# Kernel tuning notes

Measured on AMD Instinct MI355X. Metric: run time of the kernel, lower is better.

## Reference

```python
import jax, jax.numpy as jnp
import numpy as np

EPS = 1e-9
TEMP = 1.0
TOP_K = 2


def setup_inputs() -> dict:
    key = jax.random.key(0)
    k1, k2, k3, k4 = jax.random.split(key, 4)
    B, T, D, DC, E = 8, 4096, 1024, 512, 64
    din = D + DC
    inputs = jax.random.normal(k1, (B, T, D), dtype=jnp.float32)
    cond = jax.random.normal(k2, (B, T, DC), dtype=jnp.float32)
    # CondRouterMLP params (bias=False): Linear(din -> 2*din), GELU, Linear(2*din -> E)
    W1 = jax.random.normal(k3, (2 * din, din), dtype=jnp.float32) / np.sqrt(din).astype(np.float32)
    W2 = jax.random.normal(k4, (E, 2 * din), dtype=jnp.float32) / np.sqrt(2 * din).astype(np.float32)
    return {"inputs": inputs, "cond": cond, "W1": W1, "W2": W2}


def reference(inputs, cond, W1, W2):
    B, T, D = inputs.shape
    # concat hidden states with condition, flatten tokens
    x = jnp.concatenate([inputs, cond], axis=-1).reshape(-1, D + cond.shape[-1])  # [N, din]
    h = jax.nn.gelu(x @ W1.T, approximate=False)          # [N, 2*din] (torch nn.GELU = exact erf)
    logits = h @ W2.T                                     # [N, E]
    logits = (logits - logits.max(axis=-1, keepdims=True)) / TEMP
    probs = jax.nn.softmax(logits, axis=-1) + EPS
    probs = jnp.clip(probs, EPS, 1.0 - EPS)               # [N, E]
    # eval-mode top-k selection
    top_v, top_i = jax.lax.top_k(probs, TOP_K)            # [N, k]
    N, E = probs.shape
    rows = jnp.arange(N)[:, None]
    router_mask = jnp.zeros_like(probs).at[rows, top_i].set(1.0)
    router_probs = jnp.zeros_like(probs).at[rows, top_i].set(top_v)
    router_probs = router_probs / router_probs.sum(axis=-1, keepdims=True)  # normalize=True
    return (
        router_mask.reshape(B, T, E),
        top_i.reshape(B, T, TOP_K),
        router_probs.reshape(B, T, E),
        probs.reshape(B, T, E),
    )
```

## Files before the change

### kernel.cpp

```cpp
#include <hip/hip_runtime.h>
#include <cmath>

#define N_TOK 32768
#define D0    1024
#define DCC   512
#define DIN   1536
#define JD    3072
#define NE    64
#define BM    128
#define BJ    512
#define NJC   (JD/BJ)
#define NIT   48
#define NTH   512
#define HS    36
#define EPSV  1e-9f

typedef _Float16 half8 __attribute__((ext_vector_type(8)));
typedef float    f32x4 __attribute__((ext_vector_type(4)));

#define SZ_A  16384
#define SZ_B  65536
#define OFF_A 0
#define OFF_B 32768
#define LDS_TOTAL 163840
#define OFF_H    0
#define OFF_LRED 73728
#define OFF_EPI  (73728 + 34816)

#define W1N   ((size_t)JD*DIN)
#define W2N   ((size_t)NE*JD)
#define XTN   ((size_t)N_TOK*DIN)
#define XT_G  (256*192*128)
#define W1T_G (192*3072)
#define W2T_G (384*64)

__device__ __forceinline__ f32x4 mfma16(half8 a, half8 b, f32x4 c) {
    return __builtin_amdgcn_mfma_f32_16x16x32_f16(a, b, c, 0, 0, 0);
}

__device__ __forceinline__ void split8(const float4 v0, const float4 v1, half8& hh, half8& hl) {
    float f[8] = {v0.x, v0.y, v0.z, v0.w, v1.x, v1.y, v1.z, v1.w};
    #pragma unroll
    for (int i = 0; i < 8; ++i) {
        _Float16 h = (_Float16)f[i];
        hh[i] = h;
        hl[i] = (_Float16)(f[i] - (float)h);
    }
}

__device__ __forceinline__ void gload16(const void* g, void* l) {
    __builtin_amdgcn_global_load_lds(
        (const __attribute__((address_space(1))) unsigned int*)g,
        (__attribute__((address_space(3))) unsigned int*)l, 16, 0, 0);
}

__global__ void presplit_w1t(const float* __restrict__ W1,
                             _Float16* __restrict__ hi, _Float16* __restrict__ lo) {
    int g = blockIdx.x * blockDim.x + threadIdx.x;
    if (g >= W1T_G) return;
    const int j  = g % JD;
    const int ko = g / JD;
    const float* src = W1 + (size_t)j * DIN + ko * 8;
    float4 v0 = *(const float4*)src;
    float4 v1 = *(const float4*)(src + 4);
    half8 h, l;
    split8(v0, v1, h, l);
    *(half8*)(hi + (size_t)g * 8) = h;
    *(half8*)(lo + (size_t)g * 8) = l;
}

__global__ void presplit_w2t(const float* __restrict__ W2,
                             _Float16* __restrict__ hi, _Float16* __restrict__ lo) {
    int g = blockIdx.x * blockDim.x + threadIdx.x;
    if (g >= W2T_G) return;
    const int e  = g & 63;
    const int jo = g >> 6;
    const float* src = W2 + (size_t)e * JD + jo * 8;
    float4 v0 = *(const float4*)src;
    float4 v1 = *(const float4*)(src + 4);
    half8 h, l;
    split8(v0, v1, h, l);
    *(half8*)(hi + (size_t)g * 8) = h;
    *(half8*)(lo + (size_t)g * 8) = l;
}

__global__ void presplit_xt(const float* __restrict__ inp, const float* __restrict__ cnd,
                            _Float16* __restrict__ hi, _Float16* __restrict__ lo) {
    int g = blockIdx.x * blockDim.x + threadIdx.x;
    if (g >= XT_G) return;
    const int r    = g & 127;
    const int ko   = (g >> 7) % 192;
    const int tile = g / (192 * 128);
    const int token = tile * 128 + r;
    const float* src = (ko < 128) ? (inp + (size_t)token * D0 + ko * 8)
                                  : (cnd + (size_t)token * DCC + (ko - 128) * 8);
    float4 v0 = *(const float4*)src;
    float4 v1 = *(const float4*)(src + 4);
    half8 h, l;
    split8(v0, v1, h, l);
    *(half8*)(hi + (size_t)g * 8) = h;
    *(half8*)(lo + (size_t)g * 8) = l;
}

__global__ __launch_bounds__(NTH, 1)
void router_v17(const _Float16* __restrict__ Xh, const _Float16* __restrict__ Xl,
                const _Float16* __restrict__ W1h, const _Float16* __restrict__ W1l,
                const _Float16* __restrict__ W2h, const _Float16* __restrict__ W2l,
                float* __restrict__ out_mask, float* __restrict__ out_topi,
                float* __restrict__ out_rp, float* __restrict__ out_probs)
{
    __shared__ __align__(16) char smem[LDS_TOTAL];

    const int tid  = threadIdx.x;
    const int lane = tid & 63;
    const int w    = tid >> 6;
    const int tg   = w >> 2;
    const int jg   = w & 3;
    const int l15  = lane & 15;
    const int lg   = lane >> 4;
    const int blk  = blockIdx.x;
    const int t0   = blk * BM;

    const int spl = w >> 2;
    const int sko = w & 3;

    int aoff[4], boff[8];
    #pragma unroll
    for (int tf = 0; tf < 4; ++tf) aoff[tf] = (lg*128 + tg*64 + tf*16 + l15) * 16;
    #pragma unroll
    for (int jf = 0; jf < 8; ++jf) boff[jf] = lg*8192 + (jg*128 + jf*16 + l15) * 16;

    const f32x4 vzero = {0.f, 0.f, 0.f, 0.f};
    f32x4 lacc[4] = {vzero, vzero, vzero, vzero};

    const _Float16* const Wbp = spl ? W1l : W1h;
    const _Float16* const Xbp = spl ? Xl  : Xh;
    const size_t xbase = (size_t)blk * 192 * 128;

    _Float16* const myHh = (_Float16*)(smem + OFF_H + w * 9216);
    _Float16* const myHl = myHh + 2304;

    for (int jc = 0; jc < NJC; ++jc) {
        f32x4 acc1[4][8];
        #pragma unroll
        for (int tf = 0; tf < 4; ++tf)
            #pragma unroll
            for (int jf = 0; jf < 8; ++jf) acc1[tf][jf] = vzero;

        {
            const _Float16* asrc = Xbp + (xbase + (size_t)sko * 128) * 8;
            char* adst = smem + OFF_A + spl * 8192 + sko * 2048;
            gload16(asrc + (size_t)lane * 8, adst);
            gload16(asrc + (size_t)(64 + lane) * 8, adst + 1024);
            const _Float16* bsrc = Wbp + ((size_t)sko * JD + jc * BJ) * 8;
            char* bdst = smem + OFF_B + spl * 32768 + sko * 8192;
            #pragma unroll
            for (int q = 0; q < 8; ++q)
                gload16(bsrc + (size_t)(q * 64 + lane) * 8, bdst + q * 1024);
        }
        __syncthreads();

        for (int it = 0; it < NIT; ++it) {
            const int cur = it & 1, nxt = cur ^ 1;
            const bool more = (it + 1 < NIT);
            if (more) {
                const _Float16* asrc = Xbp + (xbase + (size_t)((it + 1) * 4 + sko) * 128) * 8;
                char* adst = smem + OFF_A + nxt * SZ_A + spl * 8192 + sko * 2048;
                gload16(asrc + (size_t)lane * 8, adst);
                gload16(asrc + (size_t)(64 + lane) * 8, adst + 1024);
                const _Float16* bsrc = Wbp +
                    ((size_t)((it + 1) * 4 + sko) * JD + jc * BJ) * 8;
                char* bdst = smem + OFF_B + nxt * SZ_B + spl * 32768 + sko * 8192;
                #pragma unroll
                for (int q = 0; q < 8; ++q)
                    gload16(bsrc + (size_t)(q * 64 + lane) * 8, bdst + q * 1024);
            }
            const char* ab = smem + OFF_A + cur * SZ_A;
            const char* bb = smem + OFF_B + cur * SZ_B;
            half8 ah[4], al[4];
            #pragma unroll
            for (int tf = 0; tf < 4; ++tf) {
                ah[tf] = *(const half8*)(ab + aoff[tf]);
                al[tf] = *(const half8*)(ab + 8192 + aoff[tf]);
            }
            #pragma unroll
            for (int jf = 0; jf < 8; ++jf) {
                half8 bh = *(const half8*)(bb + boff[jf]);
                half8 bl = *(const half8*)(bb + 32768 + boff[jf]);
                #pragma unroll
                for (int tf = 0; tf < 4; ++tf) {
                    acc1[tf][jf] = mfma16(ah[tf], bh, acc1[tf][jf]);
                    acc1[tf][jf] = mfma16(ah[tf], bl, acc1[tf][jf]);
                    acc1[tf][jf] = mfma16(al[tf], bh, acc1[tf][jf]);
                }
            }
            __syncthreads();
        }

        #pragma unroll
        for (int r = 0; r < 4; ++r) {
            #pragma unroll
            for (int c = 0; c < 2; ++c) {
                const int jf = 2*r + c;
                #pragma unroll
                for (int tf = 0; tf < 4; ++tf)
                    #pragma unroll
                    for (int rr = 0; rr < 4; ++rr) {
                        const float v = acc1[tf][jf][rr];
                        const float gv = 0.5f * v * (1.0f + erff(v * 0.70710678118654752f));
                        const _Float16 gh = (_Float16)gv;
                        const _Float16 gl = (_Float16)(gv - (float)gh);
                        const int o = (tf*16 + lg*4 + rr) * HS + c*16 + l15;
                        myHh[o] = gh; myHl[o] = gl;
                    }
            }
            __syncthreads();
            #pragma unroll
            for (int s = 0; s < 4; ++s) {
                const _Float16* sh = (const _Float16*)(smem + OFF_H + (tg*4 + s) * 9216);
                const _Float16* sl = sh + 2304;
                const int jo = jc*64 + s*16 + r*4 + lg;
                const size_t wg = ((size_t)jo * 64 + jg*16 + l15) * 8;
                half8 b2h = *(const half8*)(W2h + wg);
                half8 b2l = *(const half8*)(W2l + wg);
                #pragma unroll
                for (int tf = 0; tf < 4; ++tf) {
                    const int o = (tf*16 + l15) * HS + lg*8;
                    half8 a2h = *(const half8*)(sh + o);
                    half8 a2l = *(const half8*)(sl + o);
                    lacc[tf] = mfma16(a2h, b2h, lacc[tf]);
                    lacc[tf] = mfma16(a2h, b2l, lacc[tf]);
                    lacc[tf] = mfma16(a2l, b2h, lacc[tf]);
                }
            }
            __syncthreads();
        }
    }

    float* const Lred = (float*)(smem + OFF_LRED);
    #pragma unroll
    for (int tf = 0; tf < 4; ++tf)
        #pragma unroll
        for (int rr = 0; rr < 4; ++rr)
            Lred[(tg*64 + tf*16 + lg*4 + rr) * 68 + jg*16 + l15] = lacc[tf][rr];
    __syncthreads();

    float* const mA   = (float*)(smem + OFF_EPI);
    float* const invA = mA + BM;
    int*   const i1A  = (int*)(invA + BM);
    int*   const i2A  = i1A + BM;
    float* const rp1A = (float*)(i2A + BM);
    float* const rp2A = rp1A + BM;

    if (tid < BM) {
        const float* row = Lred + tid * 68;
        float m = -3.402823466e38f;
        for (int e = 0; e < NE; ++e) m = fmaxf(m, row[e]);
        float s = 0.f, v1 = -3.402823466e38f, v2 = -3.402823466e38f;
        int i1 = 0, i2 = 0;
        for (int e = 0; e < NE; ++e) {
            const float v = row[e];
            s += expf(v - m);
            if (v > v1)      { v2 = v1; i2 = i1; v1 = v; i1 = e; }
            else if (v > v2) { v2 = v; i2 = e; }
        }
        const float inv = 1.f / s;
        const float p1 = fminf(expf(v1 - m) * inv + EPSV, 1.f - EPSV);
        const float p2 = fminf(expf(v2 - m) * inv + EPSV, 1.f - EPSV);
        mA[tid] = m; invA[tid] = inv; i1A[tid] = i1; i2A[tid] = i2;
        const float den = p1 + p2;
        rp1A[tid] = p1 / den; rp2A[tid] = p2 / den;
    }
    __syncthreads();

    for (int idx = tid; idx < BM * NE; idx += NTH) {
        const int r = idx >> 6, e = idx & 63;
        const size_t o = (size_t)(t0 + r) * NE + e;
        const float p = fminf(expf(Lred[r * 68 + e] - mA[r]) * invA[r] + EPSV, 1.f - EPSV);
        const int b1 = (e == i1A[r]), b2 = (e == i2A[r]);
        out_probs[o] = p;
        out_mask[o]  = (b1 | b2) ? 1.f : 0.f;
        out_rp[o]    = b1 ? rp1A[r] : (b2 ? rp2A[r] : 0.f);
    }
    if (tid < BM * 2) {
        const int r = tid >> 1, q = tid & 1;
        out_topi[(size_t)(t0 + r) * 2 + q] = (float)(q ? i2A[r] : i1A[r]);
    }
}

#define FB_SZ_A  16384
#define FB_SZ_B  32768
#define FB_OFF_B 32768
#define FB_LDS   98304

__global__ __launch_bounds__(NTH, 1)
void router_v9fb(const float* __restrict__ inp, const float* __restrict__ cnd,
                 const _Float16* __restrict__ W1h, const _Float16* __restrict__ W1l,
                 const _Float16* __restrict__ W2h, const _Float16* __restrict__ W2l,
                 float* __restrict__ out_mask, float* __restrict__ out_topi,
                 float* __restrict__ out_rp, float* __restrict__ out_probs)
{
    __shared__ __align__(16) char smem[FB_LDS];
    const int tid  = threadIdx.x;
    const int lane = tid & 63;
    const int w    = tid >> 6;
    const int tg   = w >> 2;
    const int jg   = w & 3;
    const int l15  = lane & 15;
    const int lg   = lane >> 4;
    const int t0   = blockIdx.x * BM;
    const int akoct = w >> 1;
    const int arow  = (w & 1) * 64 + lane;
    const int bplane = w >> 2;
    const int bkoct  = w & 3;

    int aoff[4], boff[4];
    #pragma unroll
    for (int tf = 0; tf < 4; ++tf) aoff[tf] = (lg*128 + tg*64 + tf*16 + l15) * 16;
    #pragma unroll
    for (int jf = 0; jf < 4; ++jf) boff[jf] = (lg*256 + jg*64 + jf*16 + l15) * 16;

    const f32x4 vzero = {0.f, 0.f, 0.f, 0.f};
    f32x4 lacc[4] = {vzero, vzero, vzero, vzero};
    const float* const xrowA = inp + (size_t)(t0 + arow) * D0;
    const float* const xrowC = cnd + (size_t)(t0 + arow) * DCC;
    const _Float16* const Wbp = bplane ? W1l : W1h;
    _Float16* const myHh = (_Float16*)(smem + w * 9216);
    _Float16* const myHl = myHh + 2304;

    for (int jc = 0; jc < JD/256; ++jc) {
        f32x4 acc1[4][4];
        #pragma unroll
        for (int tf = 0; tf < 4; ++tf)
            #pragma unroll
            for (int jf = 0; jf < 4; ++jf) acc1[tf][jf] = vzero;
        {
            #pragma unroll
            for (int q = 0; q < 4; ++q) {
                const _Float16* src = Wbp + ((size_t)bkoct * JD + jc*256 + q*64 + lane) * 8;
                gload16(src, smem + FB_OFF_B + bplane*16384 + bkoct*4096 + q*1024);
            }
            const float* sx = xrowA + akoct * 8;
            float4 v0 = *(const float4*)sx;
            float4 v1 = *(const float4*)(sx + 4);
            half8 hh, hl;
            split8(v0, v1, hh, hl);
            const int g = (akoct*128 + arow) * 16;
            *(half8*)(smem + g) = hh;
            *(half8*)(smem + 8192 + g) = hl;
        }
        __syncthreads();
        for (int it = 0; it < NIT; ++it) {
            const int cur = it & 1, nxt = cur ^ 1;
            const bool more = (it + 1 < NIT);
            float4 xv0, xv1;
            if (more) {
                const int ko = (it + 1) * 4 + bkoct;
                #pragma unroll
                for (int q = 0; q < 4; ++q) {
                    const _Float16* src = Wbp + ((size_t)ko * JD + jc*256 + q*64 + lane) * 8;
                    gload16(src, smem + FB_OFF_B + nxt*FB_SZ_B + bplane*16384 + bkoct*4096 + q*1024);
                }
                const int k = (it + 1) * 32 + akoct * 8;
                const float* sx = (k < D0) ? (xrowA + k) : (xrowC + k - D0);
                xv0 = *(const float4*)sx;
                xv1 = *(const float4*)(sx + 4);
            }
            const char* ab = smem + cur*FB_SZ_A;
            const char* bb = smem + FB_OFF_B + cur*FB_SZ_B;
            half8 ah[4], al[4], bh[4], bl[4];
            #pragma unroll
            for (int tf = 0; tf < 4; ++tf) {
                ah[tf] = *(const half8*)(ab + aoff[tf]);
                al[tf] = *(const half8*)(ab + 8192 + aoff[tf]);
            }
            #pragma unroll
            for (int jf = 0; jf < 4; ++jf) {
                bh[jf] = *(const half8*)(bb + boff[jf]);
                bl[jf] = *(const half8*)(bb + 16384 + boff[jf]);
            }
            #pragma unroll
            for (int tf = 0; tf < 4; ++tf)
                #pragma unroll
                for (int jf = 0; jf < 4; ++jf) {
                    acc1[tf][jf] = mfma16(ah[tf], bh[jf], acc1[tf][jf]);
                    acc1[tf][jf] = mfma16(ah[tf], bl[jf], acc1[tf][jf]);
                    acc1[tf][jf] = mfma16(al[tf], bh[jf], acc1[tf][jf]);
                }
            if (more) {
                half8 hh, hl;
                split8(xv0, xv1, hh, hl);
                const int g = (akoct*128 + arow) * 16;
                *(half8*)(smem + nxt*FB_SZ_A + g) = hh;
                *(half8*)(smem + nxt*FB_SZ_A + 8192 + g) = hl;
            }
            __syncthreads();
        }
        #pragma unroll
        for (int r = 0; r < 2; ++r) {
            #pragma unroll
            for (int c = 0; c < 2; ++c) {
                const int jf = 2*r + c;
                #pragma unroll
                for (int tf = 0; tf < 4; ++tf)
                    #pragma unroll
                    for (int rr = 0; rr < 4; ++rr) {
                        const float v = acc1[tf][jf][rr];
                        const float gv = 0.5f * v * (1.0f + erff(v * 0.70710678118654752f));
                        const _Float16 gh = (_Float16)gv;
                        const _Float16 gl = (_Float16)(gv - (float)gh);
                        const int o = (tf*16 + lg*4 + rr) * HS + c*16 + l15;
                        myHh[o] = gh; myHl[o] = gl;
                    }
            }
            __syncthreads();
            #pragma unroll
            for (int s = 0; s < 4; ++s) {
                const _Float16* sh = (const _Float16*)(smem + (tg*4 + s) * 9216);
                const _Float16* sl = sh + 2304;
                const int jo = jc*32 + s*8 + r*4 + lg;
                const size_t wg = ((size_t)jo * 64 + jg*16 + l15) * 8;
                half8 b2h = *(const half8*)(W2h + wg);
                half8 b2l = *(const half8*)(W2l + wg);
                #pragma unroll
                for (int tf = 0; tf < 4; ++tf) {
                    const int o = (tf*16 + l15) * HS + lg*8;
                    half8 a2h = *(const half8*)(sh + o);
                    half8 a2l = *(const half8*)(sl + o);
                    lacc[tf] = mfma16(a2h, b2h, lacc[tf]);
                    lacc[tf] = mfma16(a2h, b2l, lacc[tf]);
                    lacc[tf] = mfma16(a2l, b2h, lacc[tf]);
                }
            }
            __syncthreads();
        }
    }
    float* const Lred = (float*)smem;
    #pragma unroll
    for (int tf = 0; tf < 4; ++tf)
        #pragma unroll
        for (int rr = 0; rr < 4; ++rr)
            Lred[(tg*64 + tf*16 + lg*4 + rr) * 68 + jg*16 + l15] = lacc[tf][rr];
    __syncthreads();
    float* const mA   = (float*)(smem + 36864);
    float* const invA = mA + BM;
    int*   const i1A  = (int*)(invA + BM);
    int*   const i2A  = i1A + BM;
    float* const rp1A = (float*)(i2A + BM);
    float* const rp2A = rp1A + BM;
    if (tid < BM) {
        const float* row = Lred + tid * 68;
        float m = -3.402823466e38f;
        for (int e = 0; e < NE; ++e) m = fmaxf(m, row[e]);
        float s = 0.f, v1 = -3.402823466e38f, v2 = -3.402823466e38f;
        int i1 = 0, i2 = 0;
        for (int e = 0; e < NE; ++e) {
            const float v = row[e];
            s += expf(v - m);
            if (v > v1)      { v2 = v1; i2 = i1; v1 = v; i1 = e; }
            else if (v > v2) { v2 = v; i2 = e; }
        }
        const float inv = 1.f / s;
        const float p1 = fminf(expf(v1 - m) * inv + EPSV, 1.f - EPSV);
        const float p2 = fminf(expf(v2 - m) * inv + EPSV, 1.f - EPSV);
        mA[tid] = m; invA[tid] = inv; i1A[tid] = i1; i2A[tid] = i2;
        const float den = p1 + p2;
        rp1A[tid] = p1 / den; rp2A[tid] = p2 / den;
    }
    __syncthreads();
    for (int idx = tid; idx < BM * NE; idx += NTH) {
        const int r = idx >> 6, e = idx & 63;
        const size_t o = (size_t)(t0 + r) * NE + e;
        const float p = fminf(expf(Lred[r * 68 + e] - mA[r]) * invA[r] + EPSV, 1.f - EPSV);
        const int b1 = (e == i1A[r]), b2 = (e == i2A[r]);
        out_probs[o] = p;
        out_mask[o]  = (b1 | b2) ? 1.f : 0.f;
        out_rp[o]    = b1 ? rp1A[r] : (b2 ? rp2A[r] : 0.f);
    }
    if (tid < BM * 2) {
        const int r = tid >> 1, q = tid & 1;
        out_topi[(size_t)(t0 + r) * 2 + q] = (float)(q ? i2A[r] : i1A[r]);
    }
}

extern "C" void kernel_launch(void* const* d_in, const int* in_sizes, int n_in,
                              void* d_out, int out_size, void* d_ws, size_t ws_size,
                              hipStream_t stream) {
    const float* inp = (const float*)d_in[0];
    const float* cnd = (const float*)d_in[1];
    const float* W1  = (const float*)d_in[2];
    const float* W2  = (const float*)d_in[3];

    float* out = (float*)d_out;
    const size_t NT = (size_t)N_TOK;
    float* out_mask  = out;
    float* out_topi  = out + NT * NE;
    float* out_rp    = out + NT * NE + NT * 2;
    float* out_probs = out + NT * NE + NT * 2 + NT * NE;

    const size_t V17_REQ = (2*XTN + 2*W1N + 2*W2N) * 2;
    if (ws_size >= V17_REQ) {
        _Float16* Xh  = (_Float16*)d_ws;
        _Float16* Xl  = Xh + XTN;
        _Float16* W1h = Xl + XTN;
        _Float16* W1l = W1h + W1N;
        _Float16* W2h = W1l + W1N;
        _Float16* W2l = W2h + W2N;
        hipLaunchKernelGGL(presplit_xt,  dim3(XT_G/256), dim3(256), 0, stream, inp, cnd, Xh, Xl);
        hipLaunchKernelGGL(presplit_w1t, dim3((W1T_G + 255)/256), dim3(256), 0, stream, W1, W1h, W1l);
        hipLaunchKernelGGL(presplit_w2t, dim3((W2T_G + 255)/256), dim3(256), 0, stream, W2, W2h, W2l);
        hipLaunchKernelGGL(router_v17, dim3(N_TOK / BM), dim3(NTH), 0, stream,
                           Xh, Xl, W1h, W1l, W2h, W2l,
                           out_mask, out_topi, out_rp, out_probs);
    } else {
        _Float16* W1h = (_Float16*)d_ws;
        _Float16* W1l = W1h + W1N;
        _Float16* W2h = W1l + W1N;
        _Float16* W2l = W2h + W2N;
        hipLaunchKernelGGL(presplit_w1t, dim3((W1T_G + 255)/256), dim3(256), 0, stream, W1, W1h, W1l);
        hipLaunchKernelGGL(presplit_w2t, dim3((W2T_G + 255)/256), dim3(256), 0, stream, W2, W2h, W2l);
        hipLaunchKernelGGL(router_v9fb, dim3(N_TOK / BM), dim3(NTH), 0, stream,
                           inp, cnd, W1h, W1l, W2h, W2l,
                           out_mask, out_topi, out_rp, out_probs);
    }
}
```

Before: 1.025 ms.

## Split hidden dimension across two blocks per tile with partial logits reduction

Adds a new router kernel that gives each 128-token tile two blocks, each handling half of the 3072 hidden columns, so 512 blocks run instead of 256 and two blocks can be resident per CU. The A operand (pre-split X) is read straight from global memory into registers instead of being staged in LDS, which cuts LDS use to 64KB. Each block writes partial logits to workspace, and a separate finishing kernel sums the two halves and does softmax/top-k. This trades extra global traffic and a kernel launch for better occupancy and CU utilization; the old fp32-input fallback kernel is removed, and v17 now runs only when the workspace is too small for the partial buffer.

```diff
diff --git a/kernel.cpp b/kernel.cpp
--- a/kernel.cpp
+++ b/kernel.cpp
@@ -9,7 +9,7 @@
 #define NE    64
 #define BM    128
 #define BJ    512
-#define NJC   (JD/BJ)
+#define NJC   6
 #define NIT   48
 #define NTH   512
 #define HS    36
@@ -17,15 +17,6 @@
 
 typedef _Float16 half8 __attribute__((ext_vector_type(8)));
 typedef float    f32x4 __attribute__((ext_vector_type(4)));
-
-#define SZ_A  16384
-#define SZ_B  65536
-#define OFF_A 0
-#define OFF_B 32768
-#define LDS_TOTAL 163840
-#define OFF_H    0
-#define OFF_LRED 73728
-#define OFF_EPI  (73728 + 34816)
 
 #define W1N   ((size_t)JD*DIN)
 #define W2N   ((size_t)NE*JD)
@@ -102,6 +93,215 @@
     *(half8*)(lo + (size_t)g * 8) = l;
 }
 
+__global__ __launch_bounds__(NTH, 2)
+void router_v19(const _Float16* __restrict__ Xh, const _Float16* __restrict__ Xl,
+                const _Float16* __restrict__ W1h, const _Float16* __restrict__ W1l,
+                const _Float16* __restrict__ W2h, const _Float16* __restrict__ W2l,
+                float* __restrict__ partial)
+{
+    __shared__ __align__(16) char smem[65536];
+
+    const int tid  = threadIdx.x;
+    const int lane = tid & 63;
+    const int w    = tid >> 6;
+    const int tg   = w >> 2;
+    const int jg   = w & 3;
+    const int l15  = lane & 15;
+    const int lg   = lane >> 4;
+    const int tile = blockIdx.x >> 1;
+    const int half = blockIdx.x & 1;
+    const int jcol0 = half * 1536;
+
+    const int bplane = w >> 2;
+    const int bkoct  = w & 3;
+
+    int boff[4];
+    #pragma unroll
+    for (int jf = 0; jf < 4; ++jf)
+        boff[jf] = (lg*256 + jg*64 + jf*16 + l15) * 16;
+
+    const _Float16* baseA[4];
+    #pragma unroll
+    for (int tf = 0; tf < 4; ++tf)
+        baseA[tf] = Xh + ((size_t)tile * 192 * 128 + tg*64 + tf*16 + l15) * 8;
+
+    const f32x4 vzero = {0.f, 0.f, 0.f, 0.f};
+    f32x4 lacc[4] = {vzero, vzero, vzero, vzero};
+
+    const _Float16* const Wbp = bplane ? W1l : W1h;
+
+    for (int jc = 0; jc < 6; ++jc) {
+        f32x4 acc1[4][4];
+        #pragma unroll
+        for (int tf = 0; tf < 4; ++tf)
+            #pragma unroll
+            for (int jf = 0; jf < 4; ++jf) acc1[tf][jf] = vzero;
+
+        {
+            const _Float16* src = Wbp + ((size_t)bkoct * JD + jcol0 + jc*256) * 8;
+            char* dst = smem + (bplane*4 + bkoct) * 4096;
+            #pragma unroll
+            for (int q = 0; q < 4; ++q)
+                gload16(src + (size_t)(q*64 + lane) * 8, dst + q * 1024);
+        }
+        __syncthreads();
+
+        for (int it = 0; it < NIT; ++it) {
+            half8 ah[4], al[4];
+            const int aoffh = (it*4 + lg) * 1024;
+            #pragma unroll
+            for (int tf = 0; tf < 4; ++tf) {
+                ah[tf] = *(const half8*)(baseA[tf] + aoffh);
+                al[tf] = *(const half8*)(baseA[tf] + XTN + aoffh);
+            }
+            __builtin_amdgcn_sched_barrier(0);
+            if (it + 1 < NIT) {
+                const _Float16* src = Wbp +
+                    ((size_t)((it+1)*4 + bkoct) * JD + jcol0 + jc*256) * 8;
+                char* dst = smem + ((it+1) & 1) * 32768 + (bplane*4 + bkoct) * 4096;
+                #pragma unroll
+                for (int q = 0; q < 4; ++q)
+                    gload16(src + (size_t)(q*64 + lane) * 8, dst + q * 1024);
+            }
+            const char* bb = smem + (it & 1) * 32768;
+            half8 bh[4], bl[4];
+            #pragma unroll
+            for (int jf = 0; jf < 4; ++jf) {
+                bh[jf] = *(const half8*)(bb + boff[jf]);
+                bl[jf] = *(const half8*)(bb + 16384 + boff[jf]);
+            }
+            #pragma unroll
+            for (int tf = 0; tf < 4; ++tf)
+                #pragma unroll
+                for (int jf = 0; jf < 4; ++jf) {
+                    acc1[tf][jf] = mfma16(ah[tf], bh[jf], acc1[tf][jf]);
+                    acc1[tf][jf] = mfma16(ah[tf], bl[jf], acc1[tf][jf]);
+                    acc1[tf][jf] = mfma16(al[tf], bh[jf], acc1[tf][jf]);
+                }
+            __syncthreads();
+        }
+
+        char* const slab = smem + w * 8192;
+        #pragma unroll
+        for (int r = 0; r < 2; ++r) {
+            #pragma unroll
+            for (int c = 0; c < 2; ++c) {
+                const int jf = 2*r + c;
+                #pragma unroll
+                for (int tf = 0; tf < 4; ++tf)
+                    #pragma unroll
+                    for (int rr = 0; rr < 4; ++rr) {
+                        const float v = acc1[tf][jf][rr];
+                        const float gv = 0.5f * v * (1.0f + erff(v * 0.70710678118654752f));
+                        const _Float16 gh = (_Float16)gv;
+                        const _Float16 gl = (_Float16)(gv - (float)gh);
+                        const int tok = tf*16 + lg*4 + rr;
+                        int ob = tok*64 + (c*16 + l15)*2;
+                        ob ^= ((tok & 3) << 4);
+                        *(_Float16*)(slab + ob) = gh;
+                        *(_Float16*)(slab + 4096 + ob) = gl;
+                    }
+            }
+            __syncthreads();
+            #pragma unroll
+            for (int s = 0; s < 4; ++s) {
+                const char* sh = smem + (tg*4 + s) * 8192;
+                const int jo = half*192 + jc*32 + s*8 + r*4 + lg;
+                const size_t wg = ((size_t)jo * 64 + jg*16 + l15) * 8;
+                half8 b2h = *(const half8*)(W2h + wg);
+                half8 b2l = *(const half8*)(W2l + wg);
+                #pragma unroll
+                for (int tf = 0; tf < 4; ++tf) {
+                    const int row = tf*16 + l15;
+                    int rb = row*64 + lg*16;
+                    rb ^= ((row & 3) << 4);
+                    half8 a2h = *(const half8*)(sh + rb);
+                    half8 a2l = *(const half8*)(sh + 4096 + rb);
+                    lacc[tf] = mfma16(a2h, b2h, lacc[tf]);
+                    lacc[tf] = mfma16(a2h, b2l, lacc[tf]);
+                    lacc[tf] = mfma16(a2l, b2h, lacc[tf]);
+                }
+            }
+            __syncthreads();
+        }
+    }
+
+    float* pp = partial + (size_t)(half*256 + tile) * 8192;
+    #pragma unroll
+    for (int tf = 0; tf < 4; ++tf)
+        #pragma unroll
+        for (int rr = 0; rr < 4; ++rr)
+            pp[(tg*64 + tf*16 + lg*4 + rr) * 64 + jg*16 + l15] = lacc[tf][rr];
+}
+
+__global__ __launch_bounds__(256, 4)
+void router_fin(const float* __restrict__ partial,
+                float* __restrict__ out_mask, float* __restrict__ out_topi,
+                float* __restrict__ out_rp, float* __restrict__ out_probs)
+{
+    __shared__ float L[128 * 68];
+    __shared__ float mA[128], invA[128], rp1A[128], rp2A[128];
+    __shared__ int   i1A[128], i2A[128];
+
+    const int tid  = threadIdx.x;
+    const int tile = blockIdx.x;
+    const int t0   = tile * 128;
+    const float4* pA = (const float4*)(partial + (size_t)tile * 8192);
+    const float4* pB = (const float4*)(partial + (size_t)(256 + tile) * 8192);
+
+    for (int idx = tid; idx < 2048; idx += 256) {
+        float4 a = pA[idx], b = pB[idx];
+        const int tok = idx >> 4, q = idx & 15;
+        float* d = &L[tok * 68 + q * 4];
+        d[0] = a.x + b.x; d[1] = a.y + b.y; d[2] = a.z + b.z; d[3] = a.w + b.w;
+    }
+    __syncthreads();
+
+    if (tid < 128) {
+        const float* row = L + tid * 68;
+        float m = -3.402823466e38f;
+        for (int e = 0; e < NE; ++e) m = fmaxf(m, row[e]);
+        float s = 0.f, v1 = -3.402823466e38f, v2 = -3.402823466e38f;
+        int i1 = 0, i2 = 0;
+        for (int e = 0; e < NE; ++e) {
+            const float v = row[e];
+            s += expf(v - m);
+            if (v > v1)      { v2 = v1; i2 = i1; v1 = v; i1 = e; }
+            else if (v > v2) { v2 = v; i2 = e; }
+        }
+        const float inv = 1.f / s;
+        const float p1 = fminf(expf(v1 - m) * inv + EPSV, 1.f - EPSV);
+        const float p2 = fminf(expf(v2 - m) * inv + EPSV, 1.f - EPSV);
+        mA[tid] = m; invA[tid] = inv; i1A[tid] = i1; i2A[tid] = i2;
+        const float den = p1 + p2;
+        rp1A[tid] = p1 / den; rp2A[tid] = p2 / den;
+    }
+    __syncthreads();
+
+    for (int idx = tid; idx < 128 * NE; idx += 256) {
+        const int r = idx >> 6, e = idx & 63;
+        const size_t o = (size_t)(t0 + r) * NE + e;
+        const float p = fminf(expf(L[r * 68 + e] - mA[r]) * invA[r] + EPSV, 1.f - EPSV);
+        const int b1 = (e == i1A[r]), b2 = (e == i2A[r]);
+        out_probs[o] = p;
+        out_mask[o]  = (b1 | b2) ? 1.f : 0.f;
+        out_rp[o]    = b1 ? rp1A[r] : (b2 ? rp2A[r] : 0.f);
+    }
+    {
+        const int r = tid >> 1, q = tid & 1;
+        out_topi[(size_t)(t0 + r) * 2 + q] = (float)(q ? i2A[r] : i1A[r]);
+    }
+}
+
+#define SZ_A  16384
+#define SZ_B  65536
+#define OFF_A 0
+#define OFF_B 32768
+#define LDS_TOTAL 163840
+#define OFF_H    0
+#define OFF_LRED 73728
+#define OFF_EPI  (73728 + 34816)
+
 __global__ __launch_bounds__(NTH, 1)
 void router_v17(const _Float16* __restrict__ Xh, const _Float16* __restrict__ Xl,
                 const _Float16* __restrict__ W1h, const _Float16* __restrict__ W1l,
@@ -288,201 +488,6 @@
     }
 }
 
-#define FB_SZ_A  16384
-#define FB_SZ_B  32768
-#define FB_OFF_B 32768
-#define FB_LDS   98304
-
-__global__ __launch_bounds__(NTH, 1)
-void router_v9fb(const float* __restrict__ inp, const float* __restrict__ cnd,
-                 const _Float16* __restrict__ W1h, const _Float16* __restrict__ W1l,
-                 const _Float16* __restrict__ W2h, const _Float16* __restrict__ W2l,
-                 float* __restrict__ out_mask, float* __restrict__ out_topi,
-                 float* __restrict__ out_rp, float* __restrict__ out_probs)
-{
-    __shared__ __align__(16) char smem[FB_LDS];
-    const int tid  = threadIdx.x;
-    const int lane = tid & 63;
-    const int w    = tid >> 6;
-    const int tg   = w >> 2;
-    const int jg   = w & 3;
-    const int l15  = lane & 15;
-    const int lg   = lane >> 4;
-    const int t0   = blockIdx.x * BM;
-    const int akoct = w >> 1;
-    const int arow  = (w & 1) * 64 + lane;
-    const int bplane = w >> 2;
-    const int bkoct  = w & 3;
-
-    int aoff[4], boff[4];
-    #pragma unroll
-    for (int tf = 0; tf < 4; ++tf) aoff[tf] = (lg*128 + tg*64 + tf*16 + l15) * 16;
-    #pragma unroll
-    for (int jf = 0; jf < 4; ++jf) boff[jf] = (lg*256 + jg*64 + jf*16 + l15) * 16;
-
-    const f32x4 vzero = {0.f, 0.f, 0.f, 0.f};
-    f32x4 lacc[4] = {vzero, vzero, vzero, vzero};
-    const float* const xrowA = inp + (size_t)(t0 + arow) * D0;
-    const float* const xrowC = cnd + (size_t)(t0 + arow) * DCC;
-    const _Float16* const Wbp = bplane ? W1l : W1h;
-    _Float16* const myHh = (_Float16*)(smem + w * 9216);
-    _Float16* const myHl = myHh + 2304;
-
-    for (int jc = 0; jc < JD/256; ++jc) {
-        f32x4 acc1[4][4];
-        #pragma unroll
-        for (int tf = 0; tf < 4; ++tf)
-            #pragma unroll
-            for (int jf = 0; jf < 4; ++jf) acc1[tf][jf] = vzero;
-        {
-            #pragma unroll
-            for (int q = 0; q < 4; ++q) {
-                const _Float16* src = Wbp + ((size_t)bkoct * JD + jc*256 + q*64 + lane) * 8;
-                gload16(src, smem + FB_OFF_B + bplane*16384 + bkoct*4096 + q*1024);
-            }
-            const float* sx = xrowA + akoct * 8;
-            float4 v0 = *(const float4*)sx;
-            float4 v1 = *(const float4*)(sx + 4);
-            half8 hh, hl;
-            split8(v0, v1, hh, hl);
-            const int g = (akoct*128 + arow) * 16;
-            *(half8*)(smem + g) = hh;
-            *(half8*)(smem + 8192 + g) = hl;
-        }
-        __syncthreads();
-        for (int it = 0; it < NIT; ++it) {
-            const int cur = it & 1, nxt = cur ^ 1;
-            const bool more = (it + 1 < NIT);
-            float4 xv0, xv1;
-            if (more) {
-                const int ko = (it + 1) * 4 + bkoct;
-                #pragma unroll
-                for (int q = 0; q < 4; ++q) {
-                    const _Float16* src = Wbp + ((size_t)ko * JD + jc*256 + q*64 + lane) * 8;
-                    gload16(src, smem + FB_OFF_B + nxt*FB_SZ_B + bplane*16384 + bkoct*4096 + q*1024);
-                }
-                const int k = (it + 1) * 32 + akoct * 8;
-                const float* sx = (k < D0) ? (xrowA + k) : (xrowC + k - D0);
-                xv0 = *(const float4*)sx;
-                xv1 = *(const float4*)(sx + 4);
-            }
-            const char* ab = smem + cur*FB_SZ_A;
-            const char* bb = smem + FB_OFF_B + cur*FB_SZ_B;
-            half8 ah[4], al[4], bh[4], bl[4];
-            #pragma unroll
-            for (int tf = 0; tf < 4; ++tf) {
-                ah[tf] = *(const half8*)(ab + aoff[tf]);
-                al[tf] = *(const half8*)(ab + 8192 + aoff[tf]);
-            }
-            #pragma unroll
-            for (int jf = 0; jf < 4; ++jf) {
-                bh[jf] = *(const half8*)(bb + boff[jf]);
-                bl[jf] = *(const half8*)(bb + 16384 + boff[jf]);
-            }
-            #pragma unroll
-            for (int tf = 0; tf < 4; ++tf)
-                #pragma unroll
-                for (int jf = 0; jf < 4; ++jf) {
-                    acc1[tf][jf] = mfma16(ah[tf], bh[jf], acc1[tf][jf]);
-                    acc1[tf][jf] = mfma16(ah[tf], bl[jf], acc1[tf][jf]);
-                    acc1[tf][jf] = mfma16(al[tf], bh[jf], acc1[tf][jf]);
-                }
-            if (more) {
-                half8 hh, hl;
-                split8(xv0, xv1, hh, hl);
-                const int g = (akoct*128 + arow) * 16;
-                *(half8*)(smem + nxt*FB_SZ_A + g) = hh;
-                *(half8*)(smem + nxt*FB_SZ_A + 8192 + g) = hl;
-            }
-            __syncthreads();
-        }
-        #pragma unroll
-        for (int r = 0; r < 2; ++r) {
-            #pragma unroll
-            for (int c = 0; c < 2; ++c) {
-                const int jf = 2*r + c;
-                #pragma unroll
-                for (int tf = 0; tf < 4; ++tf)
-                    #pragma unroll
-                    for (int rr = 0; rr < 4; ++rr) {
-                        const float v = acc1[tf][jf][rr];
-                        const float gv = 0.5f * v * (1.0f + erff(v * 0.70710678118654752f));
-                        const _Float16 gh = (_Float16)gv;
-                        const _Float16 gl = (_Float16)(gv - (float)gh);
-                        const int o = (tf*16 + lg*4 + rr) * HS + c*16 + l15;
-                        myHh[o] = gh; myHl[o] = gl;
-                    }
-            }
-            __syncthreads();
-            #pragma unroll
-            for (int s = 0; s < 4; ++s) {
-                const _Float16* sh = (const _Float16*)(smem + (tg*4 + s) * 9216);
-                const _Float16* sl = sh + 2304;
-                const int jo = jc*32 + s*8 + r*4 + lg;
-                const size_t wg = ((size_t)jo * 64 + jg*16 + l15) * 8;
-                half8 b2h = *(const half8*)(W2h + wg);
-                half8 b2l = *(const half8*)(W2l + wg);
-                #pragma unroll
-                for (int tf = 0; tf < 4; ++tf) {
-                    const int o = (tf*16 + l15) * HS + lg*8;
-                    half8 a2h = *(const half8*)(sh + o);
-                    half8 a2l = *(const half8*)(sl + o);
-                    lacc[tf] = mfma16(a2h, b2h, lacc[tf]);
-                    lacc[tf] = mfma16(a2h, b2l, lacc[tf]);
-                    lacc[tf] = mfma16(a2l, b2h, lacc[tf]);
-                }
-            }
-            __syncthreads();
-        }
-    }
-    float* const Lred = (float*)smem;
-    #pragma unroll
-    for (int tf = 0; tf < 4; ++tf)
-        #pragma unroll
-        for (int rr = 0; rr < 4; ++rr)
-            Lred[(tg*64 + tf*16 + lg*4 + rr) * 68 + jg*16 + l15] = lacc[tf][rr];
-    __syncthreads();
-    float* const mA   = (float*)(smem + 36864);
-    float* const invA = mA + BM;
-    int*   const i1A  = (int*)(invA + BM);
-    int*   const i2A  = i1A + BM;
-    float* const rp1A = (float*)(i2A + BM);
-    float* const rp2A = rp1A + BM;
-    if (tid < BM) {
-        const float* row = Lred + tid * 68;
-        float m = -3.402823466e38f;
-        for (int e = 0; e < NE; ++e) m = fmaxf(m, row[e]);
-        float s = 0.f, v1 = -3.402823466e38f, v2 = -3.402823466e38f;
-        int i1 = 0, i2 = 0;
-        for (int e = 0; e < NE; ++e) {
-            const float v = row[e];
-            s += expf(v - m);
-            if (v > v1)      { v2 = v1; i2 = i1; v1 = v; i1 = e; }
-            else if (v > v2) { v2 = v; i2 = e; }
-        }
-        const float inv = 1.f / s;
-        const float p1 = fminf(expf(v1 - m) * inv + EPSV, 1.f - EPSV);
-        const float p2 = fminf(expf(v2 - m) * inv + EPSV, 1.f - EPSV);
-        mA[tid] = m; invA[tid] = inv; i1A[tid] = i1; i2A[tid] = i2;
-        const float den = p1 + p2;
-        rp1A[tid] = p1 / den; rp2A[tid] = p2 / den;
-    }
-    __syncthreads();
-    for (int idx = tid; idx < BM * NE; idx += NTH) {
-        const int r = idx >> 6, e = idx & 63;
-        const size_t o = (size_t)(t0 + r) * NE + e;
-        const float p = fminf(expf(Lred[r * 68 + e] - mA[r]) * invA[r] + EPSV, 1.f - EPSV);
-        const int b1 = (e == i1A[r]), b2 = (e == i2A[r]);
-        out_probs[o] = p;
-        out_mask[o]  = (b1 | b2) ? 1.f : 0.f;
-        out_rp[o]    = b1 ? rp1A[r] : (b2 ? rp2A[r] : 0.f);
-    }
-    if (tid < BM * 2) {
-        const int r = tid >> 1, q = tid & 1;
-        out_topi[(size_t)(t0 + r) * 2 + q] = (float)(q ? i2A[r] : i1A[r]);
-    }
-}
-
 extern "C" void kernel_launch(void* const* d_in, const int* in_sizes, int n_in,
                               void* d_out, int out_size, void* d_ws, size_t ws_size,
                               hipStream_t stream) {
@@ -498,29 +503,28 @@
     float* out_rp    = out + NT * NE + NT * 2;
     float* out_probs = out + NT * NE + NT * 2 + NT * NE;
 
-    const size_t V17_REQ = (2*XTN + 2*W1N + 2*W2N) * 2;
-    if (ws_size >= V17_REQ) {
-        _Float16* Xh  = (_Float16*)d_ws;
-        _Float16* Xl  = Xh + XTN;
-        _Float16* W1h = Xl + XTN;
-        _Float16* W1l = W1h + W1N;
-        _Float16* W2h = W1l + W1N;
-        _Float16* W2l = W2h + W2N;
-        hipLaunchKernelGGL(presplit_xt,  dim3(XT_G/256), dim3(256), 0, stream, inp, cnd, Xh, Xl);
-        hipLaunchKernelGGL(presplit_w1t, dim3((W1T_G + 255)/256), dim3(256), 0, stream, W1, W1h, W1l);
-        hipLaunchKernelGGL(presplit_w2t, dim3((W2T_G + 255)/256), dim3(256), 0, stream, W2, W2h, W2l);
+    const size_t BASE_REQ = (2*XTN + 2*W1N + 2*W2N) * 2;
+    const size_t PART_B   = (size_t)512 * 8192 * 4;
+    _Float16* Xh  = (_Float16*)d_ws;
+    _Float16* Xl  = Xh + XTN;
+    _Float16* W1h = Xl + XTN;
+    _Float16* W1l = W1h + W1N;
+    _Float16* W2h = W1l + W1N;
+    _Float16* W2l = W2h + W2N;
+
+    hipLaunchKernelGGL(presplit_xt,  dim3(XT_G/256), dim3(256), 0, stream, inp, cnd, Xh, Xl);
+    hipLaunchKernelGGL(presplit_w1t, dim3((W1T_G + 255)/256), dim3(256), 0, stream, W1, W1h, W1l);
+    hipLaunchKernelGGL(presplit_w2t, dim3((W2T_G + 255)/256), dim3(256), 0, stream, W2, W2h, W2l);
+
+    if (ws_size >= BASE_REQ + PART_B) {
+        float* partial = (float*)((char*)d_ws + BASE_REQ);
+        hipLaunchKernelGGL(router_v19, dim3(512), dim3(NTH), 0, stream,
+                           Xh, Xl, W1h, W1l, W2h, W2l, partial);
+        hipLaunchKernelGGL(router_fin, dim3(256), dim3(256), 0, stream,
+                           partial, out_mask, out_topi, out_rp, out_probs);
+    } else {
         hipLaunchKernelGGL(router_v17, dim3(N_TOK / BM), dim3(NTH), 0, stream,
                            Xh, Xl, W1h, W1l, W2h, W2l,
                            out_mask, out_topi, out_rp, out_probs);
-    } else {
-        _Float16* W1h = (_Float16*)d_ws;
-        _Float16* W1l = W1h + W1N;
-        _Float16* W2h = W1l + W1N;
-        _Float16* W2l = W2h + W2N;
-        hipLaunchKernelGGL(presplit_w1t, dim3((W1T_G + 255)/256), dim3(256), 0, stream, W1, W1h, W1l);
-        hipLaunchKernelGGL(presplit_w2t, dim3((W2T_G + 255)/256), dim3(256), 0, stream, W2, W2h, W2l);
-        hipLaunchKernelGGL(router_v9fb, dim3(N_TOK / BM), dim3(NTH), 0, stream,
-                           inp, cnd, W1h, W1l, W2h, W2l,
-                           out_mask, out_topi, out_rp, out_probs);
-    }
-}
+    }
+}
```

New measurement: 1.088 ms. 1.06x slower.
